# Kernel optimization log

Hardware: AMD Instinct MI355X
Metric: run time of the kernel (lower is better)

The kernel has to match this reference:

```python
import jax, jax.numpy as jnp
import numpy as np

GX, GY = 512, 512   # grid_size
MAX_PT = 64         # max_pt_per_encode


def setup_inputs() -> dict:
    key = jax.random.key(0)
    k1, k2 = jax.random.split(key)
    B, N = 16, 262144
    pt_fea = jax.random.normal(k1, (B, N, 4), dtype=jnp.float32)
    xy_ind = jax.random.randint(k2, (B, N, 2), 0, GX, dtype=jnp.int32)
    return {"pt_fea": pt_fea, "xy_ind": xy_ind}


def _voxelize(fea, vid, P, S):
    # fea: [P,4] flat point features; vid: [P] linearized (batch,x,y) voxel id.
    # --- 'random' point selection: keep first MAX_PT points per voxel ---
    order = jnp.argsort(vid)                       # stable sort -> group points by voxel
    svid = vid[order]
    ar = jnp.arange(P, dtype=jnp.int32)
    change = jnp.concatenate([jnp.ones((1,), dtype=bool), svid[1:] != svid[:-1]])
    start = jax.lax.cummax(jnp.where(change, ar, 0))  # first sorted-index of each group
    rank_sorted = ar - start                          # within-group rank (grp_range_torch)
    grp_ind = jnp.zeros(P, jnp.int32).at[order].set(rank_sorted)
    remain = grp_ind < MAX_PT
    # --- scatter_max pooling of z; gather r at argmax; clamped counts ---
    z = jnp.where(remain, fea[:, 2], -jnp.inf)
    h = jax.ops.segment_max(z, vid, num_segments=S)
    cnt = jax.ops.segment_sum(remain.astype(jnp.float32), vid, num_segments=S)  # == clamp(count, max_pt)
    occ = cnt > 0
    cand = jnp.where(remain & (fea[:, 2] == h[vid]), ar, P)  # argmax via min index of max match
    argm = jax.ops.segment_min(cand, vid, num_segments=S)
    r = jnp.where(occ, fea[jnp.minimum(argm, P - 1), 3], 0.0)
    h0 = jnp.where(occ, h, 0.0)  # empty voxels stay 0 (dense zeros grid write)
    return h0, r, cnt


def reference(pt_fea, xy_ind):
    B, N, _ = pt_fea.shape
    P = B * N
    S = B * GX * GY
    fea = pt_fea.reshape(P, 4)
    b = jnp.repeat(jnp.arange(B, dtype=jnp.int32), N)
    x = xy_ind[..., 0].reshape(P).astype(jnp.int32)
    y = xy_ind[..., 1].reshape(P).astype(jnp.int32)
    vid = (b * GX + x) * GY + y
    h0, r, cnt = _voxelize(fea, vid, P, S)
    grid = jnp.stack([h0, r, cnt], axis=-1).reshape(B, GX, GY, 3)
    grid = jnp.transpose(grid, (0, 3, 1, 2))  # [B, 3, GX, GY]
    mx = grid.max(axis=(2, 3), keepdims=True)
    mn = grid.min(axis=(2, 3), keepdims=True)
    return (grid - mn) / (mx - mn)
```

## Files before the change

kernel.cpp:

```cpp
#include <hip/hip_runtime.h>
#include <stdint.h>

#define GXC 512
#define GYC 512
#define GXY (GXC * GYC)
#define NB  512
#define SC  4096
#define PT  1024
#define SPT (SC / PT)
#define LBINS 512
#define SEGB 64
#define BPB (GXY / 256)

typedef float v4f __attribute__((ext_vector_type(4)));
typedef int   v2i __attribute__((ext_vector_type(2)));

__device__ __forceinline__ unsigned f2s(float f) {
    unsigned u = __float_as_uint(f);
    return (u & 0x80000000u) ? ~u : (u | 0x80000000u);
}
__device__ __forceinline__ float s2f(unsigned u) {
    return (u & 0x80000000u) ? __uint_as_float(u ^ 0x80000000u)
                             : __uint_as_float(~u);
}
__device__ __forceinline__ unsigned long long packkey_y(float z, float r,
                                                        unsigned y) {
    return ((unsigned long long)f2s(z) << 32)
         | (unsigned long long)((f2s(r) & ~511u) | y);
}
__device__ __forceinline__ unsigned long long packkey(float z, float r) {
    return ((unsigned long long)f2s(z) << 32) | (unsigned long long)f2s(r);
}

__device__ __forceinline__ int swizzle(int g, int swz) {
    return swz ? ((g & 7) * (NB / 8) + (g >> 3)) : g;
}


__global__ __launch_bounds__(1024)
void place_kernel(const v4f* __restrict__ fea, const v2i* __restrict__ xy,
                  unsigned long long* __restrict__ keyA,
                  unsigned short* __restrict__ cnts,
                  unsigned short* __restrict__ loffs,
                  int chunk, int FPB, int swz) {
    __shared__ unsigned long long skey[SC];
    __shared__ unsigned lcnt[LBINS], loff[LBINS];
    __shared__ unsigned wsum[8];
    int t = threadIdx.x;
    int blk = swizzle(blockIdx.x, swz);
    int start = blk * chunk;

    for (int f = 0; f < FPB; ++f) {
        int fs = start + f * SC;
        if (t < LBINS) lcnt[t] = 0;
        __syncthreads();

        unsigned long long k[SPT]; unsigned lb[SPT], rk[SPT];
        #pragma unroll
        for (int kk = 0; kk < SPT; ++kk) {
            int p = fs + t + kk * PT;
            v2i q = __builtin_nontemporal_load(xy + p);
            v4f ff = __builtin_nontemporal_load(fea + p);
            k[kk]  = packkey_y(ff.z, ff.w, (unsigned)q.y);
            lb[kk] = (unsigned)q.x;
            rk[kk] = atomicAdd(&lcnt[q.x], 1u);
        }
        __syncthreads();

        unsigned c = 0, inc = 0;
        if (t < LBINS) {
            c = lcnt[t];
            inc = c;
            int lane = t & 63;
            #pragma unroll
            for (int off = 1; off < 64; off <<= 1) {
                unsigned o = __shfl_up(inc, off);
                if (lane >= off) inc += o;
            }
            if (lane == 63) wsum[t >> 6] = inc;
        }
        __syncthreads();
        if (t < 8) {
            unsigned v = wsum[t], i2 = v;
            #pragma unroll
            for (int off = 1; off < 8; off <<= 1) {
                unsigned o = __shfl_up(i2, off, 8);
                if (t >= off) i2 += o;
            }
            wsum[t] = i2 - v;
        }
        __syncthreads();
        if (t < LBINS) loff[t] = inc - c + wsum[t >> 6];
        __syncthreads();

        #pragma unroll
        for (int kk = 0; kk < SPT; ++kk)
            skey[loff[lb[kk]] + rk[kk]] = k[kk];
        __syncthreads();

        size_t seg = (size_t)blk * FPB + f;
        unsigned long long* dst = keyA + seg * SC;
        #pragma unroll
        for (int kk = 0; kk < SPT; ++kk) {
            int s = t + kk * PT;
            dst[s] = skey[s];
        }
        if (t < LBINS) {
            cnts[seg * LBINS + t]  = (unsigned short)lcnt[t];
            loffs[seg * LBINS + t] = (unsigned short)loff[t];
        }
        __syncthreads();
    }
}

__global__ __launch_bounds__(512)
void rowreduce_kernel(const unsigned long long* __restrict__ keyA,
                      const unsigned short* __restrict__ cnts,
                      const unsigned short* __restrict__ loffs,
                      float* __restrict__ out,
                      float* __restrict__ partials,
                      int bpblk, int FPB) {
    __shared__ unsigned long long sk[512];
    __shared__ unsigned scnt[512];
    __shared__ float red[8][6];
    int t = threadIdx.x;
    int bin = blockIdx.x;
    int batch = bin >> 9;
    int x = bin & (GXC - 1);
    sk[t] = 0; scnt[t] = 0;
    __syncthreads();

    int seg = t >> 3, l8 = t & 7;
    int blk = batch * bpblk + seg / FPB;
    int f = seg - (seg / FPB) * FPB;
    size_t sidx = (size_t)blk * FPB + f;
    unsigned c  = cnts[sidx * LBINS + x];
    unsigned lo = loffs[sidx * LBINS + x];
    const unsigned long long* src = keyA + sidx * SC + lo;
    for (unsigned r = l8; r < c; r += 8) {
        unsigned long long k = src[r];
        unsigned y = (unsigned)k & 511u;
        atomicMax(&sk[y], k);
        atomicAdd(&scnt[y], 1u);
    }
    __syncthreads();

    size_t ob = ((size_t)batch * 3) << 18;
    size_t xoff = (size_t)x << 9;
    unsigned cv = scnt[t];
    float h0 = 0.0f, r = 0.0f;
    if (cv) {
        unsigned long long k = sk[t];
        h0 = s2f((unsigned)(k >> 32));
        r  = s2f((unsigned)k & ~511u);
    }
    float cf = (float)cv;
    out[ob + xoff + t] = h0;
    out[ob + (size_t)(1 << 18) + xoff + t] = r;
    out[ob + (size_t)(2 << 18) + xoff + t] = cf;

    float n0 = h0, mx0 = h0, n1 = r, mx1 = r, n2 = cf, mx2 = cf;
    #pragma unroll
    for (int off = 32; off; off >>= 1) {
        n0 = fminf(n0, __shfl_down(n0, off));  mx0 = fmaxf(mx0, __shfl_down(mx0, off));
        n1 = fminf(n1, __shfl_down(n1, off));  mx1 = fmaxf(mx1, __shfl_down(mx1, off));
        n2 = fminf(n2, __shfl_down(n2, off));  mx2 = fmaxf(mx2, __shfl_down(mx2, off));
    }
    int lane = t & 63, wave = t >> 6;
    if (lane == 0) {
        red[wave][0] = n0; red[wave][1] = mx0;
        red[wave][2] = n1; red[wave][3] = mx1;
        red[wave][4] = n2; red[wave][5] = mx2;
    }
    __syncthreads();
    if (t < 6) {
        int j = t;
        float v = red[0][j];
        bool isMin = (j & 1) == 0;
        #pragma unroll
        for (int w = 1; w < 8; ++w)
            v = isMin ? fminf(v, red[w][j]) : fmaxf(v, red[w][j]);
        partials[(size_t)bin * 6 + j] = v;
    }
}

__global__ void reduce_kernel(const float* __restrict__ partials,
                              float* __restrict__ mn,
                              float* __restrict__ mx,
                              int rows) {
    int b = blockIdx.x / 6;
    int j = blockIdx.x - b * 6;
    bool isMin = (j & 1) == 0;
    float v = isMin ? INFINITY : -INFINITY;
    for (int i = threadIdx.x; i < rows; i += blockDim.x) {
        float p = partials[((size_t)b * rows + i) * 6 + j];
        v = isMin ? fminf(v, p) : fmaxf(v, p);
    }
    #pragma unroll
    for (int off = 32; off; off >>= 1) {
        float o = __shfl_down(v, off);
        v = isMin ? fminf(v, o) : fmaxf(v, o);
    }
    __shared__ float red[4];
    int lane = threadIdx.x & 63, wave = threadIdx.x >> 6;
    if (lane == 0) red[wave] = v;
    __syncthreads();
    if (threadIdx.x == 0) {
        #pragma unroll
        for (int w = 1; w < 4; ++w)
            v = isMin ? fminf(v, red[w]) : fmaxf(v, red[w]);
        int slot = b * 3 + (j >> 1);
        if (isMin) mn[slot] = v; else mx[slot] = v;
    }
}

__global__ void norm_kernel(float4* __restrict__ out,
                            const float* __restrict__ mn,
                            const float* __restrict__ mx,
                            int total4) {
    int i = blockIdx.x * blockDim.x + threadIdx.x;
    if (i >= total4) return;
    int slot = i >> 16;
    float lo = mn[slot];
    float inv = 1.0f / (mx[slot] - lo);
    float4 v = out[i];
    v.x = (v.x - lo) * inv;
    v.y = (v.y - lo) * inv;
    v.z = (v.z - lo) * inv;
    v.w = (v.w - lo) * inv;
    out[i] = v;
}

__global__ void scatter_fb(const v4f* __restrict__ fea, const v2i* __restrict__ xy,
                           unsigned long long* __restrict__ keys,
                           unsigned* __restrict__ cnt32, int N, int P) {
    int p = blockIdx.x * blockDim.x + threadIdx.x;
    if (p >= P) return;
    v2i q = __builtin_nontemporal_load(xy + p);
    v4f f = __builtin_nontemporal_load(fea + p);
    int vid = ((p / N) * GXC + q.x) * GYC + q.y;
    atomicMax(&keys[vid], packkey(f.z, f.w));
    atomicAdd(&cnt32[vid >> 2], 1u << ((vid & 3) * 8));
}

__global__ void fill_fb(const unsigned long long* __restrict__ keys,
                        const unsigned char* __restrict__ cntB,
                        float* __restrict__ out, float* __restrict__ partials) {
    int g = blockIdx.x;
    int batch = g / BPB, blkInB = g - batch * BPB;
    int rem = blkInB * 256 + threadIdx.x;
    int s = batch * GXY + rem;
    unsigned c = cntB[s];
    float h0 = 0.0f, r = 0.0f;
    if (c) {
        unsigned long long k = keys[s];
        h0 = s2f((unsigned)(k >> 32));
        r  = s2f((unsigned)(k & 0xFFFFFFFFull));
    }
    float cf = (float)c;
    size_t base = (size_t)batch * 3 * GXY + rem;
    out[base] = h0; out[base + GXY] = r; out[base + 2 * GXY] = cf;
    float n0 = h0, x0 = h0, n1 = r, x1 = r, n2 = cf, x2 = cf;
    #pragma unroll
    for (int off = 32; off; off >>= 1) {
        n0 = fminf(n0, __shfl_down(n0, off)); x0 = fmaxf(x0, __shfl_down(x0, off));
        n1 = fminf(n1, __shfl_down(n1, off)); x1 = fmaxf(x1, __shfl_down(x1, off));
        n2 = fminf(n2, __shfl_down(n2, off)); x2 = fmaxf(x2, __shfl_down(x2, off));
    }
    __shared__ float red[4][6];
    int lane = threadIdx.x & 63, wave = threadIdx.x >> 6;
    if (lane == 0) {
        red[wave][0] = n0; red[wave][1] = x0; red[wave][2] = n1;
        red[wave][3] = x1; red[wave][4] = n2; red[wave][5] = x2;
    }
    __syncthreads();
    if (threadIdx.x < 6) {
        int j = threadIdx.x;
        float v = red[0][j];
        bool isMin = (j & 1) == 0;
        #pragma unroll
        for (int w = 1; w < 4; ++w)
            v = isMin ? fminf(v, red[w][j]) : fmaxf(v, red[w][j]);
        partials[(size_t)(batch * BPB + blkInB) * 6 + j] = v;
    }
}

extern "C" void kernel_launch(void* const* d_in, const int* in_sizes, int n_in,
                              void* d_out, int out_size, void* d_ws, size_t ws_size,
                              hipStream_t stream) {
    const v4f* fea = (const v4f*)d_in[0];
    const v2i* xy  = (const v2i*)d_in[1];

    int P = in_sizes[0] / 4;
    int B = out_size / (3 * GXY);
    int N = (B > 0) ? P / B : 0;
    int S = B * GXY;
    int NBIN = B * GXC;
    int chunk = (NB > 0) ? P / NB : 0;
    int FPB = (chunk > 0) ? chunk / SC : 0;
    int bpblk = (B > 0) ? NB / B : 0;

    char* ws = (char*)d_ws;
    unsigned long long* keyA = (unsigned long long*)ws;
    size_t o = (size_t)P * 8;
    unsigned short* cnts  = (unsigned short*)(ws + o); o += (size_t)NB * FPB * LBINS * 2;
    unsigned short* loffs = (unsigned short*)(ws + o); o += (size_t)NB * FPB * LBINS * 2;
    float* partials = (float*)(ws + o);     o += (size_t)NBIN * 6 * 4;
    float* mn = (float*)(ws + o);           o += (size_t)B * 3 * 4;
    float* mx = (float*)(ws + o);           o += (size_t)B * 3 * 4;
    size_t need = o;

    int swz = (B % 8 == 0) ? 1 : 0;

    bool ok = B > 0 && P % NB == 0 && chunk % SC == 0 && N % chunk == 0
              && NB % B == 0 && bpblk * FPB == SEGB && NBIN % 256 == 0
              && ws_size >= need;

    if (ok) {
        place_kernel<<<NB, PT, 0, stream>>>(fea, xy, keyA, cnts, loffs,
                                            chunk, FPB, swz);
        rowreduce_kernel<<<NBIN, 512, 0, stream>>>(keyA, cnts, loffs,
                                                   (float*)d_out, partials,
                                                   bpblk, FPB);
        reduce_kernel<<<B * 6, 256, 0, stream>>>(partials, mn, mx, GXC);
    } else {
        float* mn_f = (float*)ws;
        float* mx_f = (float*)(ws + 256);
        float* part_f = (float*)(ws + 512);
        size_t hdr = 512 + (size_t)B * BPB * 6 * 4;
        unsigned long long* keys = (unsigned long long*)(ws + hdr);
        unsigned char* cntB = (unsigned char*)(ws + hdr + (size_t)S * 8);
        mn = mn_f; mx = mx_f;
        hipMemsetAsync(keys, 0x00, (size_t)S * 9, stream);
        scatter_fb<<<(P + 255) / 256, 256, 0, stream>>>(fea, xy, keys,
                                                        (unsigned*)cntB, N, P);
        fill_fb<<<S / 256, 256, 0, stream>>>(keys, cntB, (float*)d_out, part_f);
        reduce_kernel<<<B * 6, 256, 0, stream>>>(part_f, mn_f, mx_f, BPB);
    }
    norm_kernel<<<(out_size / 4 + 255) / 256, 256, 0, stream>>>((float4*)d_out,
                                                                mn, mx, out_size / 4);
}
```

Before: 188.5 us.

## Enlarge placement chunks and group four x-rows per rowreduce block

Each place_kernel block now sorts a single 8192-point chunk instead of looping over several 4096-point chunks. Per-bin count and offset are packed into one 32-bit meta word. rowreduce now handles four x rows per block, reading one contiguous span per segment with a single uint4 meta load, so it launches a quarter as many blocks with fewer, longer reads. norm_kernel also switches to nontemporal loads and stores. The cost is twice the shared key storage per placement block, which may lower occupancy, plus more LDS atomics per rowreduce block and a stricter fast-path condition.

```diff
diff --git a/kernel.cpp b/kernel.cpp
--- a/kernel.cpp
+++ b/kernel.cpp
@@ -5,11 +5,11 @@
 #define GYC 512
 #define GXY (GXC * GYC)
 #define NB  512
-#define SC  4096
+#define SC  8192
 #define PT  1024
 #define SPT (SC / PT)
 #define LBINS 512
-#define SEGB 64
+#define XG  4
 #define BPB (GXY / 256)
 
 typedef float v4f __attribute__((ext_vector_type(4)));
@@ -40,126 +40,124 @@
 __global__ __launch_bounds__(1024)
 void place_kernel(const v4f* __restrict__ fea, const v2i* __restrict__ xy,
                   unsigned long long* __restrict__ keyA,
-                  unsigned short* __restrict__ cnts,
-                  unsigned short* __restrict__ loffs,
-                  int chunk, int FPB, int swz) {
+                  unsigned* __restrict__ meta, int swz) {
     __shared__ unsigned long long skey[SC];
     __shared__ unsigned lcnt[LBINS], loff[LBINS];
     __shared__ unsigned wsum[8];
     int t = threadIdx.x;
     int blk = swizzle(blockIdx.x, swz);
-    int start = blk * chunk;
-
-    for (int f = 0; f < FPB; ++f) {
-        int fs = start + f * SC;
-        if (t < LBINS) lcnt[t] = 0;
-        __syncthreads();
-
-        unsigned long long k[SPT]; unsigned lb[SPT], rk[SPT];
-        #pragma unroll
-        for (int kk = 0; kk < SPT; ++kk) {
-            int p = fs + t + kk * PT;
-            v2i q = __builtin_nontemporal_load(xy + p);
-            v4f ff = __builtin_nontemporal_load(fea + p);
-            k[kk]  = packkey_y(ff.z, ff.w, (unsigned)q.y);
-            lb[kk] = (unsigned)q.x;
-            rk[kk] = atomicAdd(&lcnt[q.x], 1u);
+    int start = blk * SC;
+    if (t < LBINS) lcnt[t] = 0;
+    __syncthreads();
+
+    unsigned long long k[SPT]; unsigned lb[SPT], rk[SPT];
+    #pragma unroll
+    for (int kk = 0; kk < SPT; ++kk) {
+        int p = start + t + kk * PT;
+        v2i q = __builtin_nontemporal_load(xy + p);
+        v4f ff = __builtin_nontemporal_load(fea + p);
+        k[kk]  = packkey_y(ff.z, ff.w, (unsigned)q.y);
+        lb[kk] = (unsigned)q.x;
+        rk[kk] = atomicAdd(&lcnt[q.x], 1u);
+    }
+    __syncthreads();
+
+    unsigned c = 0, inc = 0;
+    if (t < LBINS) {
+        c = lcnt[t];
+        inc = c;
+        int lane = t & 63;
+        #pragma unroll
+        for (int off = 1; off < 64; off <<= 1) {
+            unsigned o = __shfl_up(inc, off);
+            if (lane >= off) inc += o;
         }
-        __syncthreads();
-
-        unsigned c = 0, inc = 0;
-        if (t < LBINS) {
-            c = lcnt[t];
-            inc = c;
-            int lane = t & 63;
-            #pragma unroll
-            for (int off = 1; off < 64; off <<= 1) {
-                unsigned o = __shfl_up(inc, off);
-                if (lane >= off) inc += o;
-            }
-            if (lane == 63) wsum[t >> 6] = inc;
+        if (lane == 63) wsum[t >> 6] = inc;
+    }
+    __syncthreads();
+    if (t < 8) {
+        unsigned v = wsum[t], i2 = v;
+        #pragma unroll
+        for (int off = 1; off < 8; off <<= 1) {
+            unsigned o = __shfl_up(i2, off, 8);
+            if (t >= off) i2 += o;
         }
-        __syncthreads();
-        if (t < 8) {
-            unsigned v = wsum[t], i2 = v;
-            #pragma unroll
-            for (int off = 1; off < 8; off <<= 1) {
-                unsigned o = __shfl_up(i2, off, 8);
-                if (t >= off) i2 += o;
-            }
-            wsum[t] = i2 - v;
-        }
-        __syncthreads();
-        if (t < LBINS) loff[t] = inc - c + wsum[t >> 6];
-        __syncthreads();
-
-        #pragma unroll
-        for (int kk = 0; kk < SPT; ++kk)
-            skey[loff[lb[kk]] + rk[kk]] = k[kk];
-        __syncthreads();
-
-        size_t seg = (size_t)blk * FPB + f;
-        unsigned long long* dst = keyA + seg * SC;
-        #pragma unroll
-        for (int kk = 0; kk < SPT; ++kk) {
-            int s = t + kk * PT;
-            dst[s] = skey[s];
-        }
-        if (t < LBINS) {
-            cnts[seg * LBINS + t]  = (unsigned short)lcnt[t];
-            loffs[seg * LBINS + t] = (unsigned short)loff[t];
-        }
-        __syncthreads();
-    }
+        wsum[t] = i2 - v;
+    }
+    __syncthreads();
+    if (t < LBINS) loff[t] = inc - c + wsum[t >> 6];
+    __syncthreads();
+
+    #pragma unroll
+    for (int kk = 0; kk < SPT; ++kk)
+        skey[loff[lb[kk]] + rk[kk]] = k[kk];
+    __syncthreads();
+
+    unsigned long long* dst = keyA + (size_t)blk * SC;
+    #pragma unroll
+    for (int kk = 0; kk < SPT; ++kk) {
+        int s = t + kk * PT;
+        dst[s] = skey[s];
+    }
+    if (t < LBINS)
+        meta[(size_t)blk * LBINS + t] = (loff[t] << 16) | lcnt[t];
 }
 
 __global__ __launch_bounds__(512)
 void rowreduce_kernel(const unsigned long long* __restrict__ keyA,
-                      const unsigned short* __restrict__ cnts,
-                      const unsigned short* __restrict__ loffs,
+                      const unsigned* __restrict__ meta,
                       float* __restrict__ out,
                       float* __restrict__ partials,
-                      int bpblk, int FPB) {
-    __shared__ unsigned long long sk[512];
-    __shared__ unsigned scnt[512];
+                      int bpblk) {
+    __shared__ unsigned long long sk[XG * 512];
+    __shared__ unsigned scnt[XG * 512];
     __shared__ float red[8][6];
     int t = threadIdx.x;
-    int bin = blockIdx.x;
-    int batch = bin >> 9;
-    int x = bin & (GXC - 1);
-    sk[t] = 0; scnt[t] = 0;
-    __syncthreads();
-
-    int seg = t >> 3, l8 = t & 7;
-    int blk = batch * bpblk + seg / FPB;
-    int f = seg - (seg / FPB) * FPB;
-    size_t sidx = (size_t)blk * FPB + f;
-    unsigned c  = cnts[sidx * LBINS + x];
-    unsigned lo = loffs[sidx * LBINS + x];
-    const unsigned long long* src = keyA + sidx * SC + lo;
-    for (unsigned r = l8; r < c; r += 8) {
+    int g = blockIdx.x;
+    int batch = g >> 7;
+    int xg = g & 127;
+    int x0 = xg * XG;
+    for (int i = t; i < XG * 512; i += 512) { sk[i] = 0; scnt[i] = 0; }
+    __syncthreads();
+
+    int seg = t >> 4, l16 = t & 15;
+    size_t sidx = (size_t)(batch * bpblk + seg);
+    uint4 m = *(const uint4*)(meta + sidx * LBINS + x0);
+    unsigned lo0 = m.x >> 16;
+    unsigned b1 = m.x & 0xFFFFu;
+    unsigned b2 = b1 + (m.y & 0xFFFFu);
+    unsigned b3 = b2 + (m.z & 0xFFFFu);
+    unsigned tot = b3 + (m.w & 0xFFFFu);
+    const unsigned long long* src = keyA + sidx * SC + lo0;
+    for (unsigned r = l16; r < tot; r += 16) {
         unsigned long long k = src[r];
+        int bin = (r >= b1) + (r >= b2) + (r >= b3);
         unsigned y = (unsigned)k & 511u;
-        atomicMax(&sk[y], k);
-        atomicAdd(&scnt[y], 1u);
+        atomicMax(&sk[(bin << 9) + y], k);
+        atomicAdd(&scnt[(bin << 9) + y], 1u);
     }
     __syncthreads();
 
     size_t ob = ((size_t)batch * 3) << 18;
-    size_t xoff = (size_t)x << 9;
-    unsigned cv = scnt[t];
-    float h0 = 0.0f, r = 0.0f;
-    if (cv) {
-        unsigned long long k = sk[t];
-        h0 = s2f((unsigned)(k >> 32));
-        r  = s2f((unsigned)k & ~511u);
-    }
-    float cf = (float)cv;
-    out[ob + xoff + t] = h0;
-    out[ob + (size_t)(1 << 18) + xoff + t] = r;
-    out[ob + (size_t)(2 << 18) + xoff + t] = cf;
-
-    float n0 = h0, mx0 = h0, n1 = r, mx1 = r, n2 = cf, mx2 = cf;
+    size_t xoff = (size_t)x0 << 9;
+    float n0 = INFINITY, mx0 = -INFINITY, n1 = INFINITY, mx1 = -INFINITY,
+          n2 = INFINITY, mx2 = -INFINITY;
+    for (int i = t; i < XG * 512; i += 512) {
+        unsigned cv = scnt[i];
+        float h0 = 0.0f, r = 0.0f;
+        if (cv) {
+            unsigned long long k = sk[i];
+            h0 = s2f((unsigned)(k >> 32));
+            r  = s2f((unsigned)k & ~511u);
+        }
+        float cf = (float)cv;
+        out[ob + xoff + i] = h0;
+        out[ob + (size_t)GXY + xoff + i] = r;
+        out[ob + (size_t)(2 * GXY) + xoff + i] = cf;
+        n0 = fminf(n0, h0); mx0 = fmaxf(mx0, h0);
+        n1 = fminf(n1, r);  mx1 = fmaxf(mx1, r);
+        n2 = fminf(n2, cf); mx2 = fmaxf(mx2, cf);
+    }
     #pragma unroll
     for (int off = 32; off; off >>= 1) {
         n0 = fminf(n0, __shfl_down(n0, off));  mx0 = fmaxf(mx0, __shfl_down(mx0, off));
@@ -180,7 +178,7 @@
         #pragma unroll
         for (int w = 1; w < 8; ++w)
             v = isMin ? fminf(v, red[w][j]) : fmaxf(v, red[w][j]);
-        partials[(size_t)bin * 6 + j] = v;
+        partials[(size_t)g * 6 + j] = v;
     }
 }
 
@@ -207,14 +205,14 @@
     __syncthreads();
     if (threadIdx.x == 0) {
         #pragma unroll
-        for (int w = 1; w < 4; ++w)
+        for (int w = 1; w < 4 && w < (int)(blockDim.x >> 6); ++w)
             v = isMin ? fminf(v, red[w]) : fmaxf(v, red[w]);
         int slot = b * 3 + (j >> 1);
         if (isMin) mn[slot] = v; else mx[slot] = v;
     }
 }
 
-__global__ void norm_kernel(float4* __restrict__ out,
+__global__ void norm_kernel(v4f* __restrict__ out,
                             const float* __restrict__ mn,
                             const float* __restrict__ mx,
                             int total4) {
@@ -223,12 +221,12 @@
     int slot = i >> 16;
     float lo = mn[slot];
     float inv = 1.0f / (mx[slot] - lo);
-    float4 v = out[i];
+    v4f v = __builtin_nontemporal_load(out + i);
     v.x = (v.x - lo) * inv;
     v.y = (v.y - lo) * inv;
     v.z = (v.z - lo) * inv;
     v.w = (v.w - lo) * inv;
-    out[i] = v;
+    __builtin_nontemporal_store(v, out + i);
 }
 
 __global__ void scatter_fb(const v4f* __restrict__ fea, const v2i* __restrict__ xy,
@@ -296,33 +294,28 @@
     int N = (B > 0) ? P / B : 0;
     int S = B * GXY;
     int NBIN = B * GXC;
-    int chunk = (NB > 0) ? P / NB : 0;
-    int FPB = (chunk > 0) ? chunk / SC : 0;
     int bpblk = (B > 0) ? NB / B : 0;
 
     char* ws = (char*)d_ws;
     unsigned long long* keyA = (unsigned long long*)ws;
     size_t o = (size_t)P * 8;
-    unsigned short* cnts  = (unsigned short*)(ws + o); o += (size_t)NB * FPB * LBINS * 2;
-    unsigned short* loffs = (unsigned short*)(ws + o); o += (size_t)NB * FPB * LBINS * 2;
-    float* partials = (float*)(ws + o);     o += (size_t)NBIN * 6 * 4;
+    unsigned* meta = (unsigned*)(ws + o);   o += (size_t)NB * LBINS * 4;
+    float* partials = (float*)(ws + o);     o += (size_t)(NBIN / XG) * 6 * 4;
     float* mn = (float*)(ws + o);           o += (size_t)B * 3 * 4;
     float* mx = (float*)(ws + o);           o += (size_t)B * 3 * 4;
     size_t need = o;
 
     int swz = (B % 8 == 0) ? 1 : 0;
 
-    bool ok = B > 0 && P % NB == 0 && chunk % SC == 0 && N % chunk == 0
-              && NB % B == 0 && bpblk * FPB == SEGB && NBIN % 256 == 0
-              && ws_size >= need;
+    bool ok = B > 0 && NB % B == 0 && bpblk == 32 && P == NB * SC
+              && N == bpblk * SC && ws_size >= need;
 
     if (ok) {
-        place_kernel<<<NB, PT, 0, stream>>>(fea, xy, keyA, cnts, loffs,
-                                            chunk, FPB, swz);
-        rowreduce_kernel<<<NBIN, 512, 0, stream>>>(keyA, cnts, loffs,
-                                                   (float*)d_out, partials,
-                                                   bpblk, FPB);
-        reduce_kernel<<<B * 6, 256, 0, stream>>>(partials, mn, mx, GXC);
+        place_kernel<<<NB, PT, 0, stream>>>(fea, xy, keyA, meta, swz);
+        rowreduce_kernel<<<NBIN / XG, 512, 0, stream>>>(keyA, meta,
+                                                        (float*)d_out, partials,
+                                                        bpblk);
+        reduce_kernel<<<B * 6, 256, 0, stream>>>(partials, mn, mx, GXC / XG);
     } else {
         float* mn_f = (float*)ws;
         float* mx_f = (float*)(ws + 256);
@@ -331,12 +324,12 @@
         unsigned long long* keys = (unsigned long long*)(ws + hdr);
         unsigned char* cntB = (unsigned char*)(ws + hdr + (size_t)S * 8);
         mn = mn_f; mx = mx_f;
-        hipMemsetAsync(keys, 0x00, (size_t)S * 9, stream);
+        (void)hipMemsetAsync(keys, 0x00, (size_t)S * 9, stream);
         scatter_fb<<<(P + 255) / 256, 256, 0, stream>>>(fea, xy, keys,
                                                         (unsigned*)cntB, N, P);
         fill_fb<<<S / 256, 256, 0, stream>>>(keys, cntB, (float*)d_out, part_f);
         reduce_kernel<<<B * 6, 256, 0, stream>>>(part_f, mn_f, mx_f, BPB);
     }
-    norm_kernel<<<(out_size / 4 + 255) / 256, 256, 0, stream>>>((float4*)d_out,
+    norm_kernel<<<(out_size / 4 + 255) / 256, 256, 0, stream>>>((v4f*)d_out,
                                                                 mn, mx, out_size / 4);
 }
```

Result: faster. 166.6 us (-11.6%).
